# Kernel optimization log

Hardware: AMD Instinct MI355X
Metric: run time of the kernel (lower is better)

The kernel has to match this reference:

```python
import jax, jax.numpy as jnp
import numpy as np
from jax import lax

HEADS = 8  # num_heads; also must equal cols of the input

def _conv_same(x, W, b):
    # x: (N, C_in, H, W), W: (C_out, C_in, kh, kw) -- Conv2d with padding='same'
    y = lax.conv_general_dilated(x, W, (1, 1), 'SAME',
                                 dimension_numbers=('NCHW', 'OIHW', 'NCHW'))
    return y + b[None, :, None, None]

def setup_inputs() -> dict:
    key = jax.random.key(0)
    ks = jax.random.split(key, 11)
    B, S, D, R, C = 4, 8, 512, 32, 8  # cols C == num_heads (required by the reshape)
    f = 3
    inp = {
        'q': jax.random.normal(ks[0], (B, S, D, R, C), jnp.float32),
        'k': jax.random.normal(ks[1], (B, S, D, R, C), jnp.float32),
        'v': jax.random.normal(ks[2], (B, S, D, R, C), jnp.float32),
        'Wq': jax.random.normal(ks[3], (D, D, f, f), jnp.float32) * 0.02,
        'bq': jnp.zeros((D,), jnp.float32),
        'Wk': jax.random.normal(ks[4], (D, D, f, f), jnp.float32) * 0.02,
        'bk': jnp.zeros((D,), jnp.float32),
        'Wv': jax.random.normal(ks[5], (D, D, f, f), jnp.float32) * 0.02,
        'bv': jnp.zeros((D,), jnp.float32),
        'Wo': jax.random.normal(ks[6], (D, D, f, f), jnp.float32) * 0.02,
        'bo': jnp.zeros((D,), jnp.float32),
    }
    return inp

def reference(q, k, v, Wq, bq, Wk, bk, Wv, bv, Wo, bo):
    B, S, D, R, C = q.shape
    H = HEADS
    dep = C // H  # = 1 with C == H (attention 'depth' per the original view math)

    def proj_split(x, W, b):
        y = _conv_same(x.reshape(B * S, D, R, C), W, b)          # (N, D, R, C)
        y = y.reshape(1, H, B * S, D, R, C // H)                  # raw view as in torch
        return y.transpose(0, 2, 3, 4, 1, 5)                      # (1, N, D, R, H, dep)

    q6 = proj_split(q, Wq, bq)
    k6 = proj_split(k, Wk, bk)
    v6 = proj_split(v, Wv, bv)

    # vectorized form of the per-step loop: dot over (rows, H, dep), softmax over keys
    scores = jnp.einsum('bnqrhd,bnkrhd->bnqk', q6, k6) / jnp.sqrt(jnp.float32(dep))
    attn = jax.nn.softmax(scores, axis=-1)                        # (1, N, D, D)
    out = jnp.einsum('bnqk,bnkrhd->bnqrhd', attn, v6)             # (1, N, D, R, H, dep)

    sa = out.reshape(B, S, R, H, D).transpose(0, 4, 1, 2, 3)      # (B, D, S, R, H)
    y = _conv_same(sa.reshape(B, D, S, R * H), Wo, bo)            # channels = d_model
    y = y.reshape(B, D, S, R, H)
    return y, attn
```

## Files before the change

### kernel.cpp

```cpp
#include <hip/hip_runtime.h>


typedef __attribute__((ext_vector_type(8))) short short8;
typedef __attribute__((ext_vector_type(8))) _Float16 half8;
typedef __attribute__((ext_vector_type(4))) float f32x4;
typedef __attribute__((ext_vector_type(4))) short short4v;

#define MFMA16F(a, b, c) __builtin_amdgcn_mfma_f32_16x16x32_f16((a), (b), (c), 0, 0, 0)

__device__ __forceinline__ void gl_lds16(const void* g, void* l) {
    __builtin_amdgcn_global_load_lds(
        (const __attribute__((address_space(1))) unsigned int*)g,
        (__attribute__((address_space(3))) unsigned int*)l, 16, 0, 0);
}
__device__ __forceinline__ unsigned short f2h(float f) {
    _Float16 h = (_Float16)f;
    return __builtin_bit_cast(unsigned short, h);
}

__global__ __launch_bounds__(256) void k_prep_fused(
        const float* __restrict__ q, const float* __restrict__ k,
        const float* __restrict__ v,
        const float* __restrict__ Wq, const float* __restrict__ Wk,
        const float* __restrict__ Wv, const float* __restrict__ Wo,
        unsigned short* __restrict__ Wqh, unsigned short* __restrict__ Wkh,
        unsigned short* __restrict__ Wvh, unsigned short* __restrict__ Woh,
        unsigned short* __restrict__ Xqh, unsigned short* __restrict__ Xkh,
        unsigned short* __restrict__ Xvh) {
    __shared__ __align__(16) unsigned int U[8192];
    const int b = blockIdx.x;
    const int tid = threadIdx.x;
    if (b < 1536) {
        const int cig = b & 15, n = (b >> 4) & 31, z = b >> 9;
        const float* X = z == 0 ? q : z == 1 ? k : v;
        unsigned short* Xh = z == 0 ? Xqh : z == 1 ? Xkh : Xvh;
#pragma unroll
        for (int it = 0; it < 8; ++it) {
            int ci_l = it * 4 + (tid >> 6);
            int pos = (tid & 63) * 4;
            const float4 rd =
                *(const float4*)&X[(size_t)(n * 512 + cig * 32 + ci_l) * 256 + pos];
            uint4 u;
            u.x = f2h(rd.x);
            u.y = f2h(rd.y);
            u.z = f2h(rd.z);
            u.w = f2h(rd.w);
            *(uint4*)&U[ci_l * 256 + pos] = u;
        }
        __syncthreads();
#pragma unroll
        for (int it = 0; it < 4; ++it) {
            int pos = it * 64 + (tid >> 2);
            int ci8 = (tid & 3) * 8;
            short8 h8;
#pragma unroll
            for (int j = 0; j < 8; ++j)
                h8[j] = (short)(U[(ci8 + j) * 256 + pos] & 0xffffu);
            int yy = (pos >> 3) + 1, xx = (pos & 7) + 1;
            size_t o = (size_t)((n * 34 + yy) * 10 + xx) * 512 + cig * 32 + ci8;
            *(short8*)&Xh[o] = h8;
        }
    } else if (b < 3584) {
        const int bl = b - 1536;
        const int co = bl & 511, z = bl >> 9;
        const float* W = z == 0 ? Wq : z == 1 ? Wk : z == 2 ? Wv : Wo;
        unsigned short* Wh = z == 0 ? Wqh : z == 1 ? Wkh : z == 2 ? Wvh : Woh;
        const float* Wc = W + co * 4608;
#pragma unroll
        for (int it = 0; it < 9; ++it) {
            int p = it * 256 + tid;
            float2 rd = *(const float2*)&Wc[p * 2];
            int e0 = p * 2;
            int ci0 = e0 / 9, t0 = e0 - ci0 * 9;
            U[t0 * 512 + ci0] = f2h(rd.x);
            int e1 = e0 + 1;
            int ci1 = e1 / 9, t1 = e1 - ci1 * 9;
            U[t1 * 512 + ci1] = f2h(rd.y);
        }
        __syncthreads();
        unsigned short* Whc = Wh + co * 4608;
#pragma unroll
        for (int it = 0; it < 18; ++it) {
            int j = it * 256 + tid;
            Whc[j] = (unsigned short)U[j];
        }
    } else {
        const int w = tid >> 6, l = tid & 63;
        int job = (b - 3584) * 4 + w;
        int a = job / 2688;
        int r = job - a * 2688;
        int n = r / 84;
        int ii = r - n * 84;
        unsigned short* arr = a == 0 ? Xqh : a == 1 ? Xkh : Xvh;
        int cell;
        if (ii < 11)      cell = ii;
        else if (ii < 73) { int j = ii - 11; cell = 19 + (j >> 1) * 10 + (j & 1); }
        else              cell = 329 + (ii - 73);
        short8 z8 = {0, 0, 0, 0, 0, 0, 0, 0};
        *(short8*)&arr[(size_t)(n * 340 + cell) * 512 + l * 8] = z8;
    }
}

__global__ __launch_bounds__(256) void k_conv_qkv_all(
        const unsigned short* __restrict__ Xqh, const unsigned short* __restrict__ Xkh,
        const unsigned short* __restrict__ Xvh,
        const unsigned short* __restrict__ Wqh_, const unsigned short* __restrict__ Wkh_,
        const unsigned short* __restrict__ Wvh_,
        const float* __restrict__ bq, const float* __restrict__ bk,
        const float* __restrict__ bv,
        unsigned short* __restrict__ Qh, unsigned short* __restrict__ Kh,
        unsigned short* __restrict__ Vt) {
    __shared__ __align__(16) short Ah[8192], Bh[8192];
    const int z = blockIdx.z;
    const unsigned short* Xh = z == 0 ? Xqh : z == 1 ? Xkh : Xvh;
    const unsigned short* Wh = z == 0 ? Wqh_ : z == 1 ? Wkh_ : Wvh_;
    const float* bias = z == 0 ? bq : z == 1 ? bk : bv;

    const int tid = threadIdx.x;
    const int w = tid >> 6, l = tid & 63;
    const int n   = blockIdx.x >> 1;
    const int p0  = (blockIdx.x & 1) * 128;
    const int co0 = blockIdx.y * 128;
    const int lm = l & 15, lq = l >> 4;
    const int r8 = l >> 3, c8 = (l & 7) ^ (l >> 3);

    int arow[4], brow[4];
#pragma unroll
    for (int j = 0; j < 4; ++j) {
        int rt = w * 32 + j * 8 + r8;
        int px = p0 + rt;
        int y = px >> 3, x = px & 7;
        arow[j] = ((n * 34 + y + 1) * 10 + (x + 1)) * 512 + c8 * 8;
        brow[j] = (co0 + rt) * 4608 + c8 * 8;
    }
    const int ldsW = w * 4096;

    int aoff[4][2], boff[4][2];
#pragma unroll
    for (int mi = 0; mi < 4; ++mi) {
        int row = (w & 1) * 64 + mi * 16 + lm;
#pragma unroll
        for (int ks = 0; ks < 2; ++ks)
            aoff[mi][ks] = row * 64 + ((((ks << 2) | lq) ^ (row & 7)) * 8);
    }
#pragma unroll
    for (int ni = 0; ni < 4; ++ni) {
        int row = (w >> 1) * 64 + ni * 16 + lm;
#pragma unroll
        for (int ks = 0; ks < 2; ++ks)
            boff[ni][ks] = row * 64 + ((((ks << 2) | lq) ^ (row & 7)) * 8);
    }

    f32x4 acc[4][4];
#pragma unroll
    for (int ni = 0; ni < 4; ++ni) {
        float b = bias[co0 + (w >> 1) * 64 + ni * 16 + lm];
#pragma unroll
        for (int mi = 0; mi < 4; ++mi) acc[mi][ni] = (f32x4){b, b, b, b};
    }

    for (int tap = 0; tap < 9; ++tap) {
        const int tapoff = ((tap / 3 - 1) * 10 + (tap % 3 - 1)) * 512;
        const int wb = tap * 512;
        for (int ci0 = 0; ci0 < 512; ci0 += 64) {
#pragma unroll
            for (int j = 0; j < 4; ++j)
                gl_lds16(Xh + arow[j] + tapoff + ci0, (char*)Ah + ldsW + j * 1024);
#pragma unroll
            for (int j = 0; j < 4; ++j)
                gl_lds16(Wh + brow[j] + wb + ci0, (char*)Bh + ldsW + j * 1024);
            __syncthreads();
            __builtin_amdgcn_s_setprio(1);
#pragma unroll
            for (int ks = 0; ks < 2; ++ks) {
                half8 ah[4], bh[4];
#pragma unroll
                for (int mi = 0; mi < 4; ++mi)
                    ah[mi] = *(const half8*)&Ah[aoff[mi][ks]];
#pragma unroll
                for (int ni = 0; ni < 4; ++ni)
                    bh[ni] = *(const half8*)&Bh[boff[ni][ks]];
#pragma unroll
                for (int mi = 0; mi < 4; ++mi)
#pragma unroll
                    for (int ni = 0; ni < 4; ++ni)
                        acc[mi][ni] = MFMA16F(ah[mi], bh[ni], acc[mi][ni]);
            }
            __builtin_amdgcn_s_setprio(0);
            __syncthreads();
        }
    }

    const int hh = n >> 2, nl = n & 3;
    const int pxbase = p0 + (w & 1) * 64 + lq * 4;
    const int x0q = pxbase & 7;
#pragma unroll
    for (int mi = 0; mi < 4; ++mi) {
        int px = pxbase + mi * 16;
        int y = px >> 3;
#pragma unroll
        for (int ni = 0; ni < 4; ++ni) {
            int co = co0 + (w >> 1) * 64 + ni * 16 + lm;
            int nn = nl * 8 + (co >> 6);
            int dd = (co & 63) * 8 + (y >> 2);
            int t0 = hh * 32 + (y & 3) * 8 + x0q;
            if (z < 2) {
                unsigned short* O = (z == 0) ? Qh : Kh;
                short4v hv;
#pragma unroll
                for (int r = 0; r < 4; ++r) hv[r] = (short)f2h(acc[mi][ni][r]);
                *(short4v*)&O[(nn * 512 + dd) * 256 + t0] = hv;
            } else {
#pragma unroll
                for (int r = 0; r < 4; ++r)
                    Vt[(nn * 256 + t0 + r) * 512 + dd] = f2h(acc[mi][ni][r]);
            }
        }
    }
}

__global__ __launch_bounds__(512) void k_scores_sm(
        const unsigned short* __restrict__ Qh, const unsigned short* __restrict__ Kh,
        float* __restrict__ Sc, unsigned short* __restrict__ Ph,
        uint4* __restrict__ Spz) {
    __shared__ __align__(16) short Ah[4096], Bh[32768];
    __shared__ float Mw[8][64], Sw[8][64];
    const int tid = threadIdx.x;
    const int nn = blockIdx.y, q0 = blockIdx.x * 64;

    {
        unsigned g = (blockIdx.y * 8u + blockIdx.x) * 512u + tid;
#pragma unroll
        for (int i = 0; i < 6; ++i) {
            unsigned zi = g + (unsigned)i * 131072u;
            if (zi < 660480u) Spz[zi] = (uint4){0u, 0u, 0u, 0u};
        }
    }

    const int w = tid >> 6, l = tid & 63;
    const int wq = w & 1, wk = w >> 1;
    const int lm = l & 15, lq = l >> 4;

    const int ar = tid >> 3, ac = (tid & 7) ^ ((tid >> 3) & 7);
    const int arow = (nn * 512 + q0 + ar) * 256 + ac * 8;
    int brow[8];
#pragma unroll
    for (int it = 0; it < 8; ++it) {
        int u = it * 512 + tid;
        int row = u >> 3, slot = u & 7;
        brow[it] = (nn * 512 + row) * 256 + ((slot ^ (row & 7)) * 8);
    }

    int aoff[2][2], boff[8][2];
#pragma unroll
    for (int mi = 0; mi < 2; ++mi) {
        int row = wq * 32 + mi * 16 + lm;
#pragma unroll
        for (int ks = 0; ks < 2; ++ks)
            aoff[mi][ks] = row * 64 + ((((ks << 2) | lq) ^ (row & 7)) * 8);
    }
#pragma unroll
    for (int ni = 0; ni < 8; ++ni) {
        int row = wk * 128 + ni * 16 + lm;
#pragma unroll
        for (int ks = 0; ks < 2; ++ks)
            boff[ni][ks] = row * 64 + ((((ks << 2) | lq) ^ (row & 7)) * 8);
    }

    f32x4 acc[2][8];
#pragma unroll
    for (int mi = 0; mi < 2; ++mi)
#pragma unroll
        for (int ni = 0; ni < 8; ++ni) acc[mi][ni] = (f32x4){0.f, 0.f, 0.f, 0.f};

    for (int tc = 0; tc < 256; tc += 64) {
        gl_lds16(Qh + arow + tc, (char*)Ah + (tid >> 3) * 128 + ((tid & 7) ^ ((tid >> 3) & 7)) * 16 - ((tid & 7) ^ ((tid >> 3) & 7)) * 16 + (tid & 7) * 16);
#pragma unroll
        for (int it = 0; it < 8; ++it)
            gl_lds16(Kh + brow[it] + tc, (char*)Bh + (it * 512 + tid) * 16);
        __syncthreads();
        __builtin_amdgcn_s_setprio(1);
#pragma unroll
        for (int ks = 0; ks < 2; ++ks) {
            half8 ah[2], bh[8];
#pragma unroll
            for (int mi = 0; mi < 2; ++mi) ah[mi] = *(const half8*)&Ah[aoff[mi][ks]];
#pragma unroll
            for (int ni = 0; ni < 8; ++ni) bh[ni] = *(const half8*)&Bh[boff[ni][ks]];
#pragma unroll
            for (int mi = 0; mi < 2; ++mi)
#pragma unroll
                for (int ni = 0; ni < 8; ++ni)
                    acc[mi][ni] = MFMA16F(ah[mi], bh[ni], acc[mi][ni]);
        }
        __builtin_amdgcn_s_setprio(0);
        __syncthreads();
    }

    float M[2][4];
#pragma unroll
    for (int mi = 0; mi < 2; ++mi)
#pragma unroll
        for (int r = 0; r < 4; ++r) {
            float m = acc[mi][0][r];
#pragma unroll
            for (int ni = 1; ni < 8; ++ni) m = fmaxf(m, acc[mi][ni][r]);
#pragma unroll
            for (int off = 1; off < 16; off <<= 1) m = fmaxf(m, __shfl_xor(m, off));
            M[mi][r] = m;
            if (lm == 0) Mw[w][wq * 32 + mi * 16 + lq * 4 + r] = m;
        }
    __syncthreads();
#pragma unroll
    for (int mi = 0; mi < 2; ++mi)
#pragma unroll
        for (int r = 0; r < 4; ++r) {
            int q_l = wq * 32 + mi * 16 + lq * 4 + r;
            float m = fmaxf(fmaxf(Mw[wq][q_l], Mw[wq + 2][q_l]),
                            fmaxf(Mw[wq + 4][q_l], Mw[wq + 6][q_l]));
            M[mi][r] = m;
        }
    float S[2][4];
#pragma unroll
    for (int mi = 0; mi < 2; ++mi)
#pragma unroll
        for (int r = 0; r < 4; ++r) {
            float m = M[mi][r];
            float s = 0.f;
#pragma unroll
            for (int ni = 0; ni < 8; ++ni) {
                float e = __expf(acc[mi][ni][r] - m);
                acc[mi][ni][r] = e;
                s += e;
            }
#pragma unroll
            for (int off = 1; off < 16; off <<= 1) s += __shfl_xor(s, off);
            S[mi][r] = s;
            if (lm == 0) Sw[w][wq * 32 + mi * 16 + lq * 4 + r] = s;
        }
    __syncthreads();
    float* C = Sc + nn * 262144;
    unsigned short* P = Ph + nn * 262144;
#pragma unroll
    for (int mi = 0; mi < 2; ++mi)
#pragma unroll
        for (int r = 0; r < 4; ++r) {
            int q_l = wq * 32 + mi * 16 + lq * 4 + r;
            float s = ((Sw[wq][q_l] + Sw[wq + 2][q_l]) +
                       (Sw[wq + 4][q_l] + Sw[wq + 6][q_l]));
            float inv = 1.0f / s;
            int rowbase = (q0 + q_l) * 512 + wk * 128 + lm;
#pragma unroll
            for (int ni = 0; ni < 8; ++ni) {
                float p = acc[mi][ni][r] * inv;
                C[rowbase + ni * 16] = p;
                P[rowbase + ni * 16] = f2h(p);
            }
        }
}

__global__ __launch_bounds__(256) void k_pv_mfma(
        const unsigned short* __restrict__ Ph, const unsigned short* __restrict__ Vt,
        unsigned short* __restrict__ Sp) {
    __shared__ __align__(16) short Ah[16384], Bh[8192];
    const int tid = threadIdx.x;
    const int w = tid >> 6, l = tid & 63;
    const int q0 = blockIdx.x * 128, t0 = blockIdx.y * 64, nn = blockIdx.z;
    const int lm = l & 15, lq = l >> 4;
    const int r4 = l >> 4, c16 = l & 15;

    int arow[8], brow[4];
#pragma unroll
    for (int j = 0; j < 8; ++j) {
        int rt = w * 32 + j * 4 + r4;
        arow[j] = (nn * 512 + q0 + rt) * 512 + ((c16 ^ (rt & 15)) * 8);
    }
#pragma unroll
    for (int j = 0; j < 4; ++j) {
        int rt = w * 16 + j * 4 + r4;
        brow[j] = (nn * 256 + t0 + rt) * 512 + ((c16 ^ (rt & 15)) * 8);
    }
    const int ldsA = w * 8192, ldsB = w * 4096;

    int aoff[4][4], boff[2][4];
#pragma unroll
    for (int mi = 0; mi < 4; ++mi) {
        int row = (w & 1) * 64 + mi * 16 + lm;
#pragma unroll
        for (int ks = 0; ks < 4; ++ks)
            aoff[mi][ks] = row * 128 + ((((ks << 2) | lq) ^ (row & 15)) * 8);
    }
#pragma unroll
    for (int ni = 0; ni < 2; ++ni) {
        int row = (w >> 1) * 32 + ni * 16 + lm;
#pragma unroll
        for (int ks = 0; ks < 4; ++ks)
            boff[ni][ks] = row * 128 + ((((ks << 2) | lq) ^ (row & 15)) * 8);
    }

    f32x4 acc[4][2];
#pragma unroll
    for (int mi = 0; mi < 4; ++mi)
#pragma unroll
        for (int ni = 0; ni < 2; ++ni) acc[mi][ni] = (f32x4){0.f, 0.f, 0.f, 0.f};

    for (int kc = 0; kc < 512; kc += 128) {
#pragma unroll
        for (int j = 0; j < 8; ++j)
            gl_lds16(Ph + arow[j] + kc, (char*)Ah + ldsA + j * 1024);
#pragma unroll
        for (int j = 0; j < 4; ++j)
            gl_lds16(Vt + brow[j] + kc, (char*)Bh + ldsB + j * 1024);
        __syncthreads();
#pragma unroll
        for (int ks = 0; ks < 4; ++ks) {
            half8 a[4], b[2];
#pragma unroll
            for (int mi = 0; mi < 4; ++mi) a[mi] = *(const half8*)&Ah[aoff[mi][ks]];
#pragma unroll
            for (int ni = 0; ni < 2; ++ni) b[ni] = *(const half8*)&Bh[boff[ni][ks]];
#pragma unroll
            for (int mi = 0; mi < 4; ++mi)
#pragma unroll
                for (int ni = 0; ni < 2; ++ni)
                    acc[mi][ni] = MFMA16F(a[mi], b[ni], acc[mi][ni]);
        }
        __syncthreads();
    }

    const int b2 = nn >> 3, s2 = nn & 7;
#pragma unroll
    for (int mi = 0; mi < 4; ++mi) {
        int qb = q0 + (w & 1) * 64 + lq * 4 + mi * 16;
#pragma unroll
        for (int ni = 0; ni < 2; ++ni) {
            int tc = t0 + (w >> 1) * 32 + ni * 16 + lm;
            int d2base = (tc & 31) * 8 + (tc >> 5);
#pragma unroll
            for (int r = 0; r < 4; ++r) {
                int qp = qb + r;
                int ww = (qp >> 4) * 8 + ((qp >> 1) & 7);
                int d2 = (qp & 1) * 256 + d2base;
                Sp[((b2 * 10 + s2 + 1) * 258 + ww + 1) * 512 + d2] =
                    f2h(acc[mi][ni][r]);
            }
        }
    }
}

__global__ __launch_bounds__(256) void k_conv_o_mfma(
        const unsigned short* __restrict__ Sp, const unsigned short* __restrict__ Wh,
        const float* __restrict__ bias, float* __restrict__ Y) {
    __shared__ __align__(16) short Ah[16384], Bh[8192];
    const int tid = threadIdx.x;
    const int w = tid >> 6, l = tid & 63;
    const int n   = blockIdx.x >> 4;
    const int yy  = (blockIdx.x >> 1) & 7;
    const int x0  = (blockIdx.x & 1) * 128;
    const int co0 = blockIdx.y * 64;
    const int lm = l & 15, lq = l >> 4;
    const int r4 = l >> 4, c16 = l & 15;

    int arow[8], brow[4];
#pragma unroll
    for (int j = 0; j < 8; ++j) {
        int rt = w * 32 + j * 4 + r4;
        arow[j] = ((n * 10 + yy + 1) * 258 + (x0 + rt + 1)) * 512
                  + ((c16 ^ (rt & 15)) * 8);
    }
#pragma unroll
    for (int j = 0; j < 4; ++j) {
        int rt = w * 16 + j * 4 + r4;
        brow[j] = (co0 + rt) * 4608 + ((c16 ^ (rt & 15)) * 8);
    }
    const int ldsA = w * 8192, ldsB = w * 4096;

    int aoff[4][4], boff[2][4];
#pragma unroll
    for (int mi = 0; mi < 4; ++mi) {
        int row = (w & 1) * 64 + mi * 16 + lm;
#pragma unroll
        for (int ks = 0; ks < 4; ++ks)
            aoff[mi][ks] = row * 128 + ((((ks << 2) | lq) ^ (row & 15)) * 8);
    }
#pragma unroll
    for (int ni = 0; ni < 2; ++ni) {
        int row = (w >> 1) * 32 + ni * 16 + lm;
#pragma unroll
        for (int ks = 0; ks < 4; ++ks)
            boff[ni][ks] = row * 128 + ((((ks << 2) | lq) ^ (row & 15)) * 8);
    }

    f32x4 acc[4][2];
#pragma unroll
    for (int ni = 0; ni < 2; ++ni) {
        float b = bias[co0 + (w >> 1) * 32 + ni * 16 + lm];
#pragma unroll
        for (int mi = 0; mi < 4; ++mi) acc[mi][ni] = (f32x4){b, b, b, b};
    }

    for (int tap = 0; tap < 9; ++tap) {
        const int tapoff = ((tap / 3 - 1) * 258 + (tap % 3 - 1)) * 512;
        const int wb = tap * 512;
        for (int ci0 = 0; ci0 < 512; ci0 += 128) {
#pragma unroll
            for (int j = 0; j < 8; ++j)
                gl_lds16(Sp + arow[j] + tapoff + ci0, (char*)Ah + ldsA + j * 1024);
#pragma unroll
            for (int j = 0; j < 4; ++j)
                gl_lds16(Wh + brow[j] + wb + ci0, (char*)Bh + ldsB + j * 1024);
            __syncthreads();
#pragma unroll
            for (int ks = 0; ks < 4; ++ks) {
                half8 a[4], b[2];
#pragma unroll
                for (int mi = 0; mi < 4; ++mi)
                    a[mi] = *(const half8*)&Ah[aoff[mi][ks]];
#pragma unroll
                for (int ni = 0; ni < 2; ++ni)
                    b[ni] = *(const half8*)&Bh[boff[ni][ks]];
#pragma unroll
                for (int mi = 0; mi < 4; ++mi)
#pragma unroll
                    for (int ni = 0; ni < 2; ++ni)
                        acc[mi][ni] = MFMA16F(a[mi], b[ni], acc[mi][ni]);
            }
            __syncthreads();
        }
    }

#pragma unroll
    for (int mi = 0; mi < 4; ++mi) {
        int px = x0 + (w & 1) * 64 + lq * 4 + mi * 16;
#pragma unroll
        for (int ni = 0; ni < 2; ++ni) {
            int co = co0 + (w >> 1) * 32 + ni * 16 + lm;
            *(f32x4*)&Y[n * 1048576 + co * 2048 + yy * 256 + px] = acc[mi][ni];
        }
    }
}

extern "C" void kernel_launch(void* const* d_in, const int* in_sizes, int n_in,
                              void* d_out, int out_size, void* d_ws, size_t ws_size,
                              hipStream_t stream) {
    const float* q  = (const float*)d_in[0];
    const float* k  = (const float*)d_in[1];
    const float* v  = (const float*)d_in[2];
    const float* Wq = (const float*)d_in[3];
    const float* bq = (const float*)d_in[4];
    const float* Wk = (const float*)d_in[5];
    const float* bk = (const float*)d_in[6];
    const float* Wv = (const float*)d_in[7];
    const float* bv = (const float*)d_in[8];
    const float* Wo = (const float*)d_in[9];
    const float* bo = (const float*)d_in[10];

    unsigned short* W0  = (unsigned short*)d_ws;
    unsigned short* Wqh = W0;
    unsigned short* Wkh = W0 + 2359296;
    unsigned short* Wvh = W0 + 4718592;
    unsigned short* Xvh = W0 + 7077888;
    unsigned short* Sp  = W0 + 12648448;
    unsigned short* Woh = W0 + 18219008;
    unsigned short* Qh  = W0 + 20578304;
    unsigned short* Kh  = W0 + 28966912;
    unsigned short* Vt  = W0 + 33161216;
    unsigned short* Ph = W0;

    float* y_out = (float*)d_out;
    float* attn  = y_out + 4194304;
    unsigned short* Xqh = (unsigned short*)d_out;
    unsigned short* Xkh = (unsigned short*)attn;

    k_prep_fused<<<5600, 256, 0, stream>>>(q, k, v, Wq, Wk, Wv, Wo,
                                           Wqh, Wkh, Wvh, Woh,
                                           Xqh, Xkh, Xvh);
    k_conv_qkv_all<<<dim3(64, 4, 3), 256, 0, stream>>>(
        Xqh, Xkh, Xvh, Wqh, Wkh, Wvh,
        bq, bk, bv, Qh, Kh, Vt);
    k_scores_sm<<<dim3(8, 32), 512, 0, stream>>>(Qh, Kh, attn, Ph, (uint4*)Sp);
    k_pv_mfma<<<dim3(4, 4, 32), 256, 0, stream>>>(Ph, Vt, Sp);
    k_conv_o_mfma<<<dim3(64, 8), 256, 0, stream>>>(Sp, Woh, bo, y_out);
}
```

Before: 362.2 us.

## Enlarge PV and output-conv block tiles to 512 threads with cooperative loads

The PV matmul and output convolution kernels now run 512-thread blocks with larger tiles (128x128 for PV, 256 pixels by 64 channels for the conv). Global-to-LDS loads are spread cooperatively across all threads instead of per-wave slices. MFMA sections are wrapped in s_setprio raises. The aim is to cut redundant global loads per output by reusing each staged A/B tile across more waves. In exchange there are fewer blocks in the grid, which can hurt occupancy and load balance across CUs. A redundant swizzle expression in the scores kernel is also simplified and an unused array is removed.

After: 377.9 us. +4.3%, slower.

```diff
diff --git a/kernel.cpp b/kernel.cpp
--- a/kernel.cpp
+++ b/kernel.cpp
@@ -274,7 +274,7 @@
         for (int ni = 0; ni < 8; ++ni) acc[mi][ni] = (f32x4){0.f, 0.f, 0.f, 0.f};
 
     for (int tc = 0; tc < 256; tc += 64) {
-        gl_lds16(Qh + arow + tc, (char*)Ah + (tid >> 3) * 128 + ((tid & 7) ^ ((tid >> 3) & 7)) * 16 - ((tid & 7) ^ ((tid >> 3) & 7)) * 16 + (tid & 7) * 16);
+        gl_lds16(Qh + arow + tc, (char*)Ah + tid * 16);
 #pragma unroll
         for (int it = 0; it < 8; ++it)
             gl_lds16(Kh + brow[it] + tc, (char*)Bh + (it * 512 + tid) * 16);
@@ -320,7 +320,6 @@
                             fmaxf(Mw[wq + 4][q_l], Mw[wq + 6][q_l]));
             M[mi][r] = m;
         }
-    float S[2][4];
 #pragma unroll
     for (int mi = 0; mi < 2; ++mi)
 #pragma unroll
@@ -335,7 +334,6 @@
             }
 #pragma unroll
             for (int off = 1; off < 16; off <<= 1) s += __shfl_xor(s, off);
-            S[mi][r] = s;
             if (lm == 0) Sw[w][wq * 32 + mi * 16 + lq * 4 + r] = s;
         }
     __syncthreads();
@@ -359,40 +357,37 @@
         }
 }
 
-__global__ __launch_bounds__(256) void k_pv_mfma(
+__global__ __launch_bounds__(512) void k_pv_mfma(
         const unsigned short* __restrict__ Ph, const unsigned short* __restrict__ Vt,
         unsigned short* __restrict__ Sp) {
-    __shared__ __align__(16) short Ah[16384], Bh[8192];
+    __shared__ __align__(16) short Ah[16384], Bh[16384];
     const int tid = threadIdx.x;
     const int w = tid >> 6, l = tid & 63;
-    const int q0 = blockIdx.x * 128, t0 = blockIdx.y * 64, nn = blockIdx.z;
+    const int q0 = blockIdx.x * 128, t0 = blockIdx.y * 128, nn = blockIdx.z;
+    const int wq = w & 1, wt = w >> 1;
     const int lm = l & 15, lq = l >> 4;
-    const int r4 = l >> 4, c16 = l & 15;
-
-    int arow[8], brow[4];
-#pragma unroll
-    for (int j = 0; j < 8; ++j) {
-        int rt = w * 32 + j * 4 + r4;
-        arow[j] = (nn * 512 + q0 + rt) * 512 + ((c16 ^ (rt & 15)) * 8);
-    }
+    const int sr = tid >> 4, sc = tid & 15;
+
+    int arow[4], brow[4];
 #pragma unroll
     for (int j = 0; j < 4; ++j) {
-        int rt = w * 16 + j * 4 + r4;
-        brow[j] = (nn * 256 + t0 + rt) * 512 + ((c16 ^ (rt & 15)) * 8);
-    }
-    const int ldsA = w * 8192, ldsB = w * 4096;
+        int rt = j * 32 + sr;
+        int slot = sc ^ (rt & 15);
+        arow[j] = (nn * 512 + q0 + rt) * 512 + slot * 8;
+        brow[j] = (nn * 256 + t0 + rt) * 512 + slot * 8;
+    }
 
     int aoff[4][4], boff[2][4];
 #pragma unroll
     for (int mi = 0; mi < 4; ++mi) {
-        int row = (w & 1) * 64 + mi * 16 + lm;
+        int row = wq * 64 + mi * 16 + lm;
 #pragma unroll
         for (int ks = 0; ks < 4; ++ks)
             aoff[mi][ks] = row * 128 + ((((ks << 2) | lq) ^ (row & 15)) * 8);
     }
 #pragma unroll
     for (int ni = 0; ni < 2; ++ni) {
-        int row = (w >> 1) * 32 + ni * 16 + lm;
+        int row = wt * 32 + ni * 16 + lm;
 #pragma unroll
         for (int ks = 0; ks < 4; ++ks)
             boff[ni][ks] = row * 128 + ((((ks << 2) | lq) ^ (row & 15)) * 8);
@@ -406,12 +401,13 @@
 
     for (int kc = 0; kc < 512; kc += 128) {
 #pragma unroll
-        for (int j = 0; j < 8; ++j)
-            gl_lds16(Ph + arow[j] + kc, (char*)Ah + ldsA + j * 1024);
-#pragma unroll
         for (int j = 0; j < 4; ++j)
-            gl_lds16(Vt + brow[j] + kc, (char*)Bh + ldsB + j * 1024);
+            gl_lds16(Ph + arow[j] + kc, (char*)Ah + (j * 512 + tid) * 16);
+#pragma unroll
+        for (int j = 0; j < 4; ++j)
+            gl_lds16(Vt + brow[j] + kc, (char*)Bh + (j * 512 + tid) * 16);
         __syncthreads();
+        __builtin_amdgcn_s_setprio(1);
 #pragma unroll
         for (int ks = 0; ks < 4; ++ks) {
             half8 a[4], b[2];
@@ -425,16 +421,17 @@
                 for (int ni = 0; ni < 2; ++ni)
                     acc[mi][ni] = MFMA16F(a[mi], b[ni], acc[mi][ni]);
         }
+        __builtin_amdgcn_s_setprio(0);
         __syncthreads();
     }
 
     const int b2 = nn >> 3, s2 = nn & 7;
 #pragma unroll
     for (int mi = 0; mi < 4; ++mi) {
-        int qb = q0 + (w & 1) * 64 + lq * 4 + mi * 16;
+        int qb = q0 + wq * 64 + lq * 4 + mi * 16;
 #pragma unroll
         for (int ni = 0; ni < 2; ++ni) {
-            int tc = t0 + (w >> 1) * 32 + ni * 16 + lm;
+            int tc = t0 + wt * 32 + ni * 16 + lm;
             int d2base = (tc & 31) * 8 + (tc >> 5);
 #pragma unroll
             for (int r = 0; r < 4; ++r) {
@@ -448,44 +445,44 @@
     }
 }
 
-__global__ __launch_bounds__(256) void k_conv_o_mfma(
+__global__ __launch_bounds__(512) void k_conv_o_mfma(
         const unsigned short* __restrict__ Sp, const unsigned short* __restrict__ Wh,
         const float* __restrict__ bias, float* __restrict__ Y) {
-    __shared__ __align__(16) short Ah[16384], Bh[8192];
+    __shared__ __align__(16) short Ah[32768], Bh[8192];
     const int tid = threadIdx.x;
     const int w = tid >> 6, l = tid & 63;
-    const int n   = blockIdx.x >> 4;
-    const int yy  = (blockIdx.x >> 1) & 7;
-    const int x0  = (blockIdx.x & 1) * 128;
+    const int n   = blockIdx.x >> 3;
+    const int yy  = blockIdx.x & 7;
     const int co0 = blockIdx.y * 64;
+    const int wp = w & 3, wc = w >> 2;
     const int lm = l & 15, lq = l >> 4;
-    const int r4 = l >> 4, c16 = l & 15;
-
-    int arow[8], brow[4];
+    const int sr = tid >> 4, sc = tid & 15;
+
+    int arow[8], brow[2];
 #pragma unroll
     for (int j = 0; j < 8; ++j) {
-        int rt = w * 32 + j * 4 + r4;
-        arow[j] = ((n * 10 + yy + 1) * 258 + (x0 + rt + 1)) * 512
-                  + ((c16 ^ (rt & 15)) * 8);
-    }
-#pragma unroll
-    for (int j = 0; j < 4; ++j) {
-        int rt = w * 16 + j * 4 + r4;
-        brow[j] = (co0 + rt) * 4608 + ((c16 ^ (rt & 15)) * 8);
-    }
-    const int ldsA = w * 8192, ldsB = w * 4096;
+        int rt = j * 32 + sr;
+        int slot = sc ^ (rt & 15);
+        arow[j] = ((n * 10 + yy + 1) * 258 + (rt + 1)) * 512 + slot * 8;
+    }
+#pragma unroll
+    for (int j = 0; j < 2; ++j) {
+        int rt = j * 32 + sr;
+        int slot = sc ^ (rt & 15);
+        brow[j] = (co0 + rt) * 4608 + slot * 8;
+    }
 
     int aoff[4][4], boff[2][4];
 #pragma unroll
     for (int mi = 0; mi < 4; ++mi) {
-        int row = (w & 1) * 64 + mi * 16 + lm;
+        int row = wp * 64 + mi * 16 + lm;
 #pragma unroll
         for (int ks = 0; ks < 4; ++ks)
             aoff[mi][ks] = row * 128 + ((((ks << 2) | lq) ^ (row & 15)) * 8);
     }
 #pragma unroll
     for (int ni = 0; ni < 2; ++ni) {
-        int row = (w >> 1) * 32 + ni * 16 + lm;
+        int row = wc * 32 + ni * 16 + lm;
 #pragma unroll
         for (int ks = 0; ks < 4; ++ks)
             boff[ni][ks] = row * 128 + ((((ks << 2) | lq) ^ (row & 15)) * 8);
@@ -494,7 +491,7 @@
     f32x4 acc[4][2];
 #pragma unroll
     for (int ni = 0; ni < 2; ++ni) {
-        float b = bias[co0 + (w >> 1) * 32 + ni * 16 + lm];
+        float b = bias[co0 + wc * 32 + ni * 16 + lm];
 #pragma unroll
         for (int mi = 0; mi < 4; ++mi) acc[mi][ni] = (f32x4){b, b, b, b};
     }
@@ -505,11 +502,14 @@
         for (int ci0 = 0; ci0 < 512; ci0 += 128) {
 #pragma unroll
             for (int j = 0; j < 8; ++j)
-                gl_lds16(Sp + arow[j] + tapoff + ci0, (char*)Ah + ldsA + j * 1024);
-#pragma unroll
-            for (int j = 0; j < 4; ++j)
-                gl_lds16(Wh + brow[j] + wb + ci0, (char*)Bh + ldsB + j * 1024);
+                gl_lds16(Sp + arow[j] + tapoff + ci0,
+                         (char*)Ah + (j * 512 + tid) * 16);
+#pragma unroll
+            for (int j = 0; j < 2; ++j)
+                gl_lds16(Wh + brow[j] + wb + ci0,
+                         (char*)Bh + (j * 512 + tid) * 16);
             __syncthreads();
+            __builtin_amdgcn_s_setprio(1);
 #pragma unroll
             for (int ks = 0; ks < 4; ++ks) {
                 half8 a[4], b[2];
@@ -525,16 +525,17 @@
                     for (int ni = 0; ni < 2; ++ni)
                         acc[mi][ni] = MFMA16F(a[mi], b[ni], acc[mi][ni]);
             }
+            __builtin_amdgcn_s_setprio(0);
             __syncthreads();
         }
     }
 
 #pragma unroll
     for (int mi = 0; mi < 4; ++mi) {
-        int px = x0 + (w & 1) * 64 + lq * 4 + mi * 16;
+        int px = wp * 64 + lq * 4 + mi * 16;
 #pragma unroll
         for (int ni = 0; ni < 2; ++ni) {
-            int co = co0 + (w >> 1) * 32 + ni * 16 + lm;
+            int co = co0 + wc * 32 + ni * 16 + lm;
             *(f32x4*)&Y[n * 1048576 + co * 2048 + yy * 256 + px] = acc[mi][ni];
         }
     }
@@ -579,6 +580,6 @@
         Xqh, Xkh, Xvh, Wqh, Wkh, Wvh,
         bq, bk, bv, Qh, Kh, Vt);
     k_scores_sm<<<dim3(8, 32), 512, 0, stream>>>(Qh, Kh, attn, Ph, (uint4*)Sp);
-    k_pv_mfma<<<dim3(4, 4, 32), 256, 0, stream>>>(Ph, Vt, Sp);
-    k_conv_o_mfma<<<dim3(64, 8), 256, 0, stream>>>(Sp, Woh, bo, y_out);
-}
+    k_pv_mfma<<<dim3(4, 2, 32), 512, 0, stream>>>(Ph, Vt, Sp);
+    k_conv_o_mfma<<<dim3(32, 8), 512, 0, stream>>>(Sp, Woh, bo, y_out);
+}
```
